# Kernel optimization log

Measured on AMD Instinct MI355X. Metric: run time of the kernel, lower is better.

The kernel has to match this reference:

```python
import jax, jax.numpy as jnp
import numpy as np

S, B, E, H, L = 256, 64, 512, 512, 4

def setup_inputs() -> dict:
    key = jax.random.key(0)
    k1, k2, k3 = jax.random.split(key, 3)
    x = jax.random.normal(k1, (S, B, E), dtype=jnp.float32)
    W_i = jax.random.normal(k2, (L, 4 * H, E), dtype=jnp.float32) * 0.1
    W_h = jax.random.normal(k3, (L, 4 * H, H), dtype=jnp.float32) * 0.1
    b = jnp.zeros((L, 4 * H), dtype=jnp.float32)
    return {"x": x, "W_i": W_i, "W_h": W_h, "b": b}


def _run_dir(xs, Wi, Wh, bb, reverse):
    """One LSTM direction over time. xs: [S,B,in]. Returns (hs [S,B,H], h_last)."""
    hidden = Wh.shape[-1]
    batch = xs.shape[1]
    # Precompute input contribution for all timesteps (batched GEMM):
    pre = jnp.einsum('sbe,ge->sbg', xs, Wi) + bb  # [S,B,4H], gates (i,f,o,g)

    def cell(carry, px):
        h, c = carry
        z = px + h @ Wh.T  # [B,4H]
        i, f, o, g = jnp.split(z, 4, axis=-1)
        i = jax.nn.sigmoid(i)
        f = jax.nn.sigmoid(f)
        o = jax.nn.sigmoid(o)
        g = jnp.tanh(g)
        c = f * c + i * g
        h = o * jnp.tanh(c)
        return (h, c), h

    h0 = jnp.zeros((batch, hidden), dtype=xs.dtype)
    (h_last, _), hs = jax.lax.scan(cell, (h0, h0), pre, reverse=reverse)
    # reverse=True scans t=S-1..0 but places outputs at original indices,
    # matching the torch code's bwd_outputs[t] assignment.
    return hs, h_last


def reference(x, W_i, W_h, b):
    layer_in = x
    hf = hb = None
    n_layers = W_i.shape[0]
    for l in range(n_layers):
        hs_f, hf = _run_dir(layer_in, W_i[l], W_h[l], b[l], reverse=False)
        hs_b, hb = _run_dir(layer_in, W_i[l], W_h[l], b[l], reverse=True)  # shared weights
        layer_in = hs_f + hs_b  # module sums directions (dropout p=0.0 is identity)
    return layer_in, hf + hb
```

## Files before the change

### kernel.cpp

```cpp
#include <hip/hip_runtime.h>
#include <math.h>

#define S_  256
#define B_  64
#define E_  512
#define H_  512
#define G4_ 2048
#define NL_ 4
#define E4_ 128

typedef __attribute__((ext_vector_type(8))) _Float16 f16x8;
typedef __attribute__((ext_vector_type(4))) float f32x4;

__device__ __forceinline__ float fsigmoid(float x) {
    return 1.0f / (1.0f + __expf(-x));
}
__device__ __forceinline__ float ftanh_(float x) {
    x = fminf(fmaxf(x, -15.0f), 15.0f);
    float e = __expf(2.0f * x);
    return (e - 1.0f) / (e + 1.0f);
}
__device__ __forceinline__ ushort f2h(float x) {
    _Float16 h = (_Float16)x;
    return *(ushort*)&h;
}
__device__ __forceinline__ float h2f(ushort u) {
    _Float16 h = *(_Float16*)&u;
    return (float)h;
}

__device__ __forceinline__ void dma16(const ushort* g, ushort* l) {
    __builtin_amdgcn_global_load_lds(
        (const __attribute__((address_space(1))) unsigned*)g,
        (__attribute__((address_space(3))) unsigned*)l, 16, 0, 0);
}

#define SLAB_ ((size_t)16 * 512)
__device__ __forceinline__ size_t slab_off(int t, int grp) {
    return (size_t)(t * 8 + grp) * SLAB_;
}


__global__ __launch_bounds__(256) void wif_k(
    const float* __restrict__ Wi, ushort* __restrict__ WiF)
{
    int i = blockIdx.x * 256 + threadIdx.x;
    int nt = i >> 10, ks = (i >> 6) & 15, l = i & 63;
    int n = nt * 16 + (l & 15);
    int k = ks * 32 + ((l >> 4) << 3);
    const float* src = Wi + (size_t)n * E_ + k;
    float4 v0 = *(const float4*)src, v1 = *(const float4*)(src + 4);
    ushort o[8] = {f2h(v0.x), f2h(v0.y), f2h(v0.z), f2h(v0.w),
                   f2h(v1.x), f2h(v1.y), f2h(v1.z), f2h(v1.w)};
    *(ushort4*)(WiF + (size_t)i * 8)     = *(ushort4*)&o[0];
    *(ushort4*)(WiF + (size_t)i * 8 + 4) = *(ushort4*)&o[4];
}

__global__ __launch_bounds__(256) void whf_k(
    const float* __restrict__ Wh, ushort* __restrict__ WhF)
{
    int i = blockIdx.x * 256 + threadIdx.x;
    int e = i & 7, l = (i >> 3) & 63, ks = (i >> 9) & 15;
    int w = (i >> 13) & 3, wgin = i >> 15;
    int r = l & 15, g = r & 3, j = wgin * 16 + w * 4 + (r >> 2);
    int k = ks * 32 + ((l >> 4) << 3) + e;
    WhF[i] = f2h(Wh[(size_t)(g * H_ + j) * H_ + k]);
}

__global__ __launch_bounds__(256) void cvt_x_k(
    const float* __restrict__ x, ushort* __restrict__ inF)
{
    int i = blockIdx.x * 256 + threadIdx.x;
    int mt = i >> 10, ks = (i >> 6) & 15, l = i & 63;
    int m = mt * 16 + (l & 15);
    int k = ks * 32 + ((l >> 4) << 3);
    const float* src = x + (size_t)m * E_ + k;
    float4 v0 = *(const float4*)src, v1 = *(const float4*)(src + 4);
    ushort o[8] = {f2h(v0.x), f2h(v0.y), f2h(v0.z), f2h(v0.w),
                   f2h(v1.x), f2h(v1.y), f2h(v1.z), f2h(v1.w)};
    *(ushort4*)(inF + (size_t)i * 8)     = *(ushort4*)&o[0];
    *(ushort4*)(inF + (size_t)i * 8 + 4) = *(ushort4*)&o[4];
}

__global__ __launch_bounds__(256) void cvt_hs_k(
    const ushort* __restrict__ hb, ushort* __restrict__ inF)
{
    int i = blockIdx.x * 256 + threadIdx.x;
    int mt = i >> 10, ks = (i >> 6) & 15, l = i & 63;
    int m = mt * 16 + (l & 15);
    int k = ks * 32 + ((l >> 4) << 3);
    int t = m >> 6, b = m & 63, cc = b & 15, bb = b >> 4;
    const ushort* pF = hb + slab_off(t, bb * 2 + 0) + (size_t)cc * 512 + k;
    const ushort* pB = hb + slab_off(t, bb * 2 + 1) + (size_t)cc * 512 + k;
    ushort4 f0 = *(const ushort4*)pF, f1 = *(const ushort4*)(pF + 4);
    ushort4 b0 = *(const ushort4*)pB, b1 = *(const ushort4*)(pB + 4);
    ushort o[8] = {f2h(h2f(f0.x) + h2f(b0.x)), f2h(h2f(f0.y) + h2f(b0.y)),
                   f2h(h2f(f0.z) + h2f(b0.z)), f2h(h2f(f0.w) + h2f(b0.w)),
                   f2h(h2f(f1.x) + h2f(b1.x)), f2h(h2f(f1.y) + h2f(b1.y)),
                   f2h(h2f(f1.z) + h2f(b1.z)), f2h(h2f(f1.w) + h2f(b1.w))};
    *(ushort4*)(inF + (size_t)i * 8)     = *(ushort4*)&o[0];
    *(ushort4*)(inF + (size_t)i * 8 + 4) = *(ushort4*)&o[4];
}

__global__ __launch_bounds__(256) void gemm_mfma_k(
    const ushort* __restrict__ WiF,
    const ushort* __restrict__ inF,
    const float* __restrict__ bias,
    float* __restrict__ pre)
{
    const int tid = threadIdx.x;
    const int w   = tid >> 6;
    const int l   = tid & 63;
    const int nb  = blockIdx.x >> 6;
    const int mb  = blockIdx.x & 63;

    f32x4 acc[4][4];
#pragma unroll
    for (int i = 0; i < 4; ++i)
#pragma unroll
        for (int j = 0; j < 4; ++j) acc[i][j] = f32x4{0.f, 0.f, 0.f, 0.f};

    const ushort* aB = WiF + ((size_t)(nb * 4) * 16) * 512 + l * 8;
    const ushort* bB = inF + ((size_t)(mb * 16 + w * 4) * 16) * 512 + l * 8;

    for (int ks = 0; ks < 16; ++ks) {
        f16x8 af[4], bf[4];
#pragma unroll
        for (int i = 0; i < 4; ++i)
            af[i] = *(const f16x8*)(aB + ((size_t)i * 16 + ks) * 512);
#pragma unroll
        for (int j = 0; j < 4; ++j)
            bf[j] = *(const f16x8*)(bB + ((size_t)j * 16 + ks) * 512);
#pragma unroll
        for (int i = 0; i < 4; ++i)
#pragma unroll
            for (int j = 0; j < 4; ++j)
                acc[i][j] = __builtin_amdgcn_mfma_f32_16x16x32_f16(
                    af[i], bf[j], acc[i][j], 0, 0, 0);
    }

#pragma unroll
    for (int i = 0; i < 4; ++i) {
#pragma unroll
        for (int j = 0; j < 4; ++j) {
#pragma unroll
            for (int g = 0; g < 4; ++g) {
                int n = nb * 64 + i * 16 + ((l >> 4) << 2) + g;
                int m = mb * 256 + w * 64 + j * 16 + (l & 15);
                int t = m >> 6, b = m & 63;
                pre[((size_t)t * G4_ + n) * B_ + b] = acc[i][j][g] + bias[n];
            }
        }
    }
}

__global__ __launch_bounds__(256, 1) void lstm_persist_k(
    const float* __restrict__ pre,
    const ushort* __restrict__ WhF,
    ushort* __restrict__ hb,
    unsigned* __restrict__ flg)
{
    __shared__ ushort hS[8192];

    const int tid  = threadIdx.x;
    const int grp  = blockIdx.x & 7;
    const int wgin = blockIdx.x >> 3;
    const int dir  = grp & 1;
    const int bblk = grp >> 1;
    const int w    = tid >> 6;
    const int l    = tid & 63;
    const int ch   = l & 15;
    const int jloc = l >> 4;
    const int j    = wgin * 16 + w * 4 + jloc;
    const int b    = bblk * 16 + ch;

    const ushort* wbase = WhF + ((size_t)(wgin * 4 + w) << 13) + (l << 3);
    const int dmaLane = (l & 15) * 512 + ((l >> 4) << 3);

    f16x8 wF[16];
#pragma unroll
    for (int ks = 0; ks < 16; ++ks)
        wF[ks] = *(const f16x8*)(wbase + (ks << 9));

    float c = 0.0f;

    for (int t = 0; t < S_; ++t) {
#pragma unroll
        for (int ks = 0; ks < 16; ++ks)
            asm volatile("" : "+v"(wF[ks]));

        const int tf = dir ? (S_ - 1 - t) : t;

        f32x4 acc;
#pragma unroll
        for (int g = 0; g < 4; ++g)
            acc[g] = pre[((size_t)tf * G4_ + g * H_ + j) * B_ + b];

        if (t > 0) {
            const unsigned* fb = &flg[((size_t)grp * S_ + (t - 1)) * 32];
            unsigned guard = 0;
            for (;;) {
                unsigned f = __hip_atomic_load(&fb[l & 31], __ATOMIC_RELAXED,
                                               __HIP_MEMORY_SCOPE_AGENT);
                if (__all(f != 0)) break;
                if (++guard > (1u << 18)) break;
            }

            const int tfp = dir ? (tf + 1) : (tf - 1);
            const ushort* slab = hb + slab_off(tfp, grp);
#pragma unroll
            for (int i = 0; i < 4; ++i) {
                int ks = (w << 2) + i;
                dma16(slab + ks * 32 + dmaLane, hS + ks * 512);
            }
            asm volatile("s_waitcnt vmcnt(0)" ::: "memory");
            __syncthreads();

            f32x4 a1 = {0.f, 0.f, 0.f, 0.f};
#pragma unroll
            for (int ks = 0; ks < 16; ks += 2) {
                f16x8 b0 = *(const f16x8*)&hS[(ks << 9) + (l << 3)];
                f16x8 b1 = *(const f16x8*)&hS[((ks + 1) << 9) + (l << 3)];
                acc = __builtin_amdgcn_mfma_f32_16x16x32_f16(wF[ks], b0, acc, 0, 0, 0);
                a1  = __builtin_amdgcn_mfma_f32_16x16x32_f16(wF[ks + 1], b1, a1, 0, 0, 0);
            }
#pragma unroll
            for (int g = 0; g < 4; ++g) acc[g] += a1[g];
        }

        float si = fsigmoid(acc[0]);
        float sf = fsigmoid(acc[1]);
        float so = fsigmoid(acc[2]);
        float tg = ftanh_(acc[3]);
        c = fmaf(sf, c, si * tg);
        float h = so * ftanh_(c);

        unsigned hv = f2h(h);
        unsigned pv = (unsigned)__shfl_xor((int)hv, 16);
        if ((jloc & 1) == 0) {
            unsigned pair = (hv & 0xFFFFu) | (pv << 16);
            unsigned* shW = (unsigned*)(hb + slab_off(tf, grp));
            __hip_atomic_store(&shW[(size_t)ch * 256 + (j >> 1)], pair,
                               __ATOMIC_RELAXED, __HIP_MEMORY_SCOPE_AGENT);
        }
        asm volatile("s_waitcnt vmcnt(0)" ::: "memory");
        __syncthreads();
        if (tid == 0)
            __hip_atomic_store(&flg[((size_t)grp * S_ + t) * 32 + wgin], 1u,
                               __ATOMIC_RELAXED, __HIP_MEMORY_SCOPE_AGENT);
    }
}

__global__ __launch_bounds__(256) void t4_to_row_k(
    const ushort* __restrict__ hb, float* __restrict__ out)
{
    int i  = blockIdx.x * 256 + threadIdx.x;
    int e4 = i & (E4_ - 1);
    int b  = (i >> 7) & 63;
    int t  = i >> 13;
    int cc = b & 15, bb = b >> 4;
    size_t e = (size_t)cc * 512 + e4 * 4;
    ushort4 hF = *(const ushort4*)(hb + slab_off(t, bb * 2 + 0) + e);
    ushort4 hB = *(const ushort4*)(hb + slab_off(t, bb * 2 + 1) + e);
    float4 v = make_float4(h2f(hF.x) + h2f(hB.x), h2f(hF.y) + h2f(hB.y),
                           h2f(hF.z) + h2f(hB.z), h2f(hF.w) + h2f(hB.w));
    *(float4*)&out[((size_t)(t * B_ + b)) * E_ + e4 * 4] = v;
}

__global__ __launch_bounds__(256) void tail_k(
    const ushort* __restrict__ hb, float* __restrict__ out2)
{
    int i = blockIdx.x * 256 + threadIdx.x;
    int b = i >> 9, j = i & 511;
    int cc = b & 15, bb = b >> 4;
    ushort hF = hb[slab_off(255, bb * 2 + 0) + (size_t)cc * 512 + j];
    ushort hB = hb[slab_off(0,   bb * 2 + 1) + (size_t)cc * 512 + j];
    out2[i] = h2f(hF) + h2f(hB);
}

extern "C" void kernel_launch(void* const* d_in, const int* in_sizes, int n_in,
                              void* d_out, int out_size, void* d_ws, size_t ws_size,
                              hipStream_t stream) {
    const float* x    = (const float*)d_in[0];
    const float* Wi   = (const float*)d_in[1];
    const float* Wh   = (const float*)d_in[2];
    const float* bias = (const float*)d_in[3];
    float* out = (float*)d_out;

    float* ws  = (float*)d_ws;
    float* pre = ws;
    ushort* hb = (ushort*)(pre + (size_t)S_ * G4_ * B_);
    unsigned* flg = (unsigned*)(hb + (size_t)S_ * 8 * SLAB_);
    ushort* WhF = (ushort*)(flg + (size_t)8 * S_ * 32);
    ushort* WiF = WhF + (size_t)1024 * 1024;
    ushort* inF = WiF + (size_t)1024 * 1024;

    for (int l = 0; l < NL_; ++l) {
        const float* wi_l = Wi + (size_t)l * G4_ * E_;
        const float* wh_l = Wh + (size_t)l * G4_ * H_;
        const float* b_l  = bias + (size_t)l * G4_;
        if (l == 0) cvt_x_k<<<4096, 256, 0, stream>>>(x, inF);
        else        cvt_hs_k<<<4096, 256, 0, stream>>>(hb, inF);
        wif_k<<<512, 256, 0, stream>>>(wi_l, WiF);
        gemm_mfma_k<<<2048, 256, 0, stream>>>(WiF, inF, b_l, pre);
        whf_k<<<4096, 256, 0, stream>>>(wh_l, WhF);
        hipMemsetAsync(flg, 0, (size_t)8 * S_ * 32 * sizeof(unsigned), stream);
        lstm_persist_k<<<256, 256, 0, stream>>>(pre, WhF, hb, flg);
    }
    t4_to_row_k<<<8192, 256, 0, stream>>>(hb, out);
    tail_k<<<128, 256, 0, stream>>>(hb, out + (size_t)S_ * B_ * H_);
}
```

Before: 3.317 ms.

## Replace flag-based step sync with canary-poll on h slabs, drop LDS staging

The per-step flag array and its barrier and flag store are removed. The h buffer is now pre-filled with a canary pattern, and each wave polls its own fragment of the previous step's h directly from global memory into registers, using cache-bypassing loads, until no canary words remain. The LDS DMA staging and __syncthreads per step are dropped, and weight conversions for all layers are hoisted into one upfront loop. The aim is to shorten the per-step critical path. The cost is a memset of the whole h buffer each layer and repeated 16-load polls. Correctness relies on 0x7C7C never being a real f16 output, which holds since 0x7C7C is a NaN encoding.

```diff
diff --git a/kernel.cpp b/kernel.cpp
--- a/kernel.cpp
+++ b/kernel.cpp
@@ -11,6 +11,9 @@
 
 typedef __attribute__((ext_vector_type(8))) _Float16 f16x8;
 typedef __attribute__((ext_vector_type(4))) float f32x4;
+typedef __attribute__((ext_vector_type(4))) unsigned u32x4;
+
+#define CANARY_ 0x7C7C7C7Cu
 
 __device__ __forceinline__ float fsigmoid(float x) {
     return 1.0f / (1.0f + __expf(-x));
@@ -27,12 +30,6 @@
 __device__ __forceinline__ float h2f(ushort u) {
     _Float16 h = *(_Float16*)&u;
     return (float)h;
-}
-
-__device__ __forceinline__ void dma16(const ushort* g, ushort* l) {
-    __builtin_amdgcn_global_load_lds(
-        (const __attribute__((address_space(1))) unsigned*)g,
-        (__attribute__((address_space(3))) unsigned*)l, 16, 0, 0);
 }
 
 #define SLAB_ ((size_t)16 * 512)
@@ -157,11 +154,8 @@
 __global__ __launch_bounds__(256, 1) void lstm_persist_k(
     const float* __restrict__ pre,
     const ushort* __restrict__ WhF,
-    ushort* __restrict__ hb,
-    unsigned* __restrict__ flg)
-{
-    __shared__ ushort hS[8192];
-
+    ushort* __restrict__ hb)
+{
     const int tid  = threadIdx.x;
     const int grp  = blockIdx.x & 7;
     const int wgin = blockIdx.x >> 3;
@@ -175,7 +169,7 @@
     const int b    = bblk * 16 + ch;
 
     const ushort* wbase = WhF + ((size_t)(wgin * 4 + w) << 13) + (l << 3);
-    const int dmaLane = (l & 15) * 512 + ((l >> 4) << 3);
+    const int fragLane = (l & 15) * 512 + ((l >> 4) << 3);
 
     f16x8 wF[16];
 #pragma unroll
@@ -197,32 +191,34 @@
             acc[g] = pre[((size_t)tf * G4_ + g * H_ + j) * B_ + b];
 
         if (t > 0) {
-            const unsigned* fb = &flg[((size_t)grp * S_ + (t - 1)) * 32];
+            const int tfp = dir ? (tf + 1) : (tf - 1);
+            const ushort* src = hb + slab_off(tfp, grp) + fragLane;
+
+            f16x8 u[16];
             unsigned guard = 0;
             for (;;) {
-                unsigned f = __hip_atomic_load(&fb[l & 31], __ATOMIC_RELAXED,
-                                               __HIP_MEMORY_SCOPE_AGENT);
-                if (__all(f != 0)) break;
+#pragma unroll
+                for (int ks = 0; ks < 16; ++ks)
+                    asm volatile("global_load_dwordx4 %0, %1, off sc0 sc1"
+                                 : "=v"(u[ks]) : "v"(src + ks * 32));
+                asm volatile("s_waitcnt vmcnt(0)" ::: "memory");
+                __builtin_amdgcn_sched_barrier(0);
+                unsigned dirty = 0;
+#pragma unroll
+                for (int ks = 0; ks < 16; ++ks) {
+                    u32x4 v = __builtin_bit_cast(u32x4, u[ks]);
+                    dirty |= (v[0] == CANARY_) | (v[1] == CANARY_) |
+                             (v[2] == CANARY_) | (v[3] == CANARY_);
+                }
+                if (!__any(dirty)) break;
                 if (++guard > (1u << 18)) break;
             }
 
-            const int tfp = dir ? (tf + 1) : (tf - 1);
-            const ushort* slab = hb + slab_off(tfp, grp);
-#pragma unroll
-            for (int i = 0; i < 4; ++i) {
-                int ks = (w << 2) + i;
-                dma16(slab + ks * 32 + dmaLane, hS + ks * 512);
-            }
-            asm volatile("s_waitcnt vmcnt(0)" ::: "memory");
-            __syncthreads();
-
             f32x4 a1 = {0.f, 0.f, 0.f, 0.f};
 #pragma unroll
             for (int ks = 0; ks < 16; ks += 2) {
-                f16x8 b0 = *(const f16x8*)&hS[(ks << 9) + (l << 3)];
-                f16x8 b1 = *(const f16x8*)&hS[((ks + 1) << 9) + (l << 3)];
-                acc = __builtin_amdgcn_mfma_f32_16x16x32_f16(wF[ks], b0, acc, 0, 0, 0);
-                a1  = __builtin_amdgcn_mfma_f32_16x16x32_f16(wF[ks + 1], b1, a1, 0, 0, 0);
+                acc = __builtin_amdgcn_mfma_f32_16x16x32_f16(wF[ks], u[ks], acc, 0, 0, 0);
+                a1  = __builtin_amdgcn_mfma_f32_16x16x32_f16(wF[ks + 1], u[ks + 1], a1, 0, 0, 0);
             }
 #pragma unroll
             for (int g = 0; g < 4; ++g) acc[g] += a1[g];
@@ -243,11 +239,6 @@
             __hip_atomic_store(&shW[(size_t)ch * 256 + (j >> 1)], pair,
                                __ATOMIC_RELAXED, __HIP_MEMORY_SCOPE_AGENT);
         }
-        asm volatile("s_waitcnt vmcnt(0)" ::: "memory");
-        __syncthreads();
-        if (tid == 0)
-            __hip_atomic_store(&flg[((size_t)grp * S_ + t) * 32 + wgin], 1u,
-                               __ATOMIC_RELAXED, __HIP_MEMORY_SCOPE_AGENT);
     }
 }
 
@@ -289,23 +280,26 @@
 
     float* ws  = (float*)d_ws;
     float* pre = ws;
-    ushort* hb = (ushort*)(pre + (size_t)S_ * G4_ * B_);
-    unsigned* flg = (unsigned*)(hb + (size_t)S_ * 8 * SLAB_);
-    ushort* WhF = (ushort*)(flg + (size_t)8 * S_ * 32);
-    ushort* WiF = WhF + (size_t)1024 * 1024;
-    ushort* inF = WiF + (size_t)1024 * 1024;
+    ushort* hb   = (ushort*)(pre + (size_t)S_ * G4_ * B_);
+    ushort* WhF4 = hb + (size_t)S_ * 8 * SLAB_;
+    ushort* WiF4 = WhF4 + (size_t)4 * 1024 * 1024;
+    ushort* inF  = WiF4 + (size_t)4 * 1024 * 1024;
 
     for (int l = 0; l < NL_; ++l) {
-        const float* wi_l = Wi + (size_t)l * G4_ * E_;
-        const float* wh_l = Wh + (size_t)l * G4_ * H_;
-        const float* b_l  = bias + (size_t)l * G4_;
+        whf_k<<<4096, 256, 0, stream>>>(Wh + (size_t)l * G4_ * H_,
+                                        WhF4 + (size_t)l * 1024 * 1024);
+        wif_k<<<512, 256, 0, stream>>>(Wi + (size_t)l * G4_ * E_,
+                                       WiF4 + (size_t)l * 1024 * 1024);
+    }
+
+    for (int l = 0; l < NL_; ++l) {
         if (l == 0) cvt_x_k<<<4096, 256, 0, stream>>>(x, inF);
         else        cvt_hs_k<<<4096, 256, 0, stream>>>(hb, inF);
-        wif_k<<<512, 256, 0, stream>>>(wi_l, WiF);
-        gemm_mfma_k<<<2048, 256, 0, stream>>>(WiF, inF, b_l, pre);
-        whf_k<<<4096, 256, 0, stream>>>(wh_l, WhF);
-        hipMemsetAsync(flg, 0, (size_t)8 * S_ * 32 * sizeof(unsigned), stream);
-        lstm_persist_k<<<256, 256, 0, stream>>>(pre, WhF, hb, flg);
+        gemm_mfma_k<<<2048, 256, 0, stream>>>(WiF4 + (size_t)l * 1024 * 1024,
+                                              inF, bias + (size_t)l * G4_, pre);
+        hipMemsetAsync(hb, 0x7C, (size_t)S_ * 8 * SLAB_ * sizeof(ushort), stream);
+        lstm_persist_k<<<256, 256, 0, stream>>>(
+            pre, WhF4 + (size_t)l * 1024 * 1024, hb);
     }
     t4_to_row_k<<<8192, 256, 0, stream>>>(hb, out);
     tail_k<<<128, 256, 0, stream>>>(hb, out + (size_t)S_ * B_ * H_);
```

After: 10.61 ms. +219.8%, slower.
